# Kernel tuning notes

Measured on AMD Instinct MI355X. Metric: run time of the kernel, lower is better.

## Reference

```python
import jax, jax.numpy as jnp
import numpy as np
from jax import lax

B, C_IN, H, W = 16, 256, 64, 64
C_OUT, K_SZ, N_EXP, RED_C = 256, 3, 4, 16  # reduction_channels = max(256//16,16)=16


def setup_inputs() -> dict:
    key = jax.random.key(0)
    ks = jax.random.split(key, 6)
    x = jax.random.normal(ks[0], (B, C_IN, H, W), dtype=jnp.float32)
    # routing network params (1x1 convs == dense on pooled features)
    w1 = jax.random.normal(ks[1], (RED_C, C_IN), dtype=jnp.float32) * (1.0 / np.sqrt(C_IN))
    b1 = jnp.zeros((RED_C,), dtype=jnp.float32)
    w2 = jax.random.normal(ks[2], (N_EXP * C_IN, RED_C), dtype=jnp.float32) * (1.0 / np.sqrt(RED_C))
    b2 = jnp.zeros((N_EXP * C_IN,), dtype=jnp.float32)
    # expert weight bank (num_experts, c_out, c_in, kh, kw)
    fan_in = C_IN * K_SZ * K_SZ
    bound = np.sqrt(6.0 / fan_in)  # kaiming_uniform with a=sqrt(5) ~ U(-sqrt(6/fan_in)*..., simplified scale)
    weight = jax.random.uniform(ks[3], (N_EXP, C_OUT, C_IN, K_SZ, K_SZ), dtype=jnp.float32, minval=-bound, maxval=bound)
    return {"x": x, "w1": w1, "b1": b1, "w2": w2, "b2": b2, "weight": weight}


def reference(x, w1, b1, w2, b2, weight):
    b = x.shape[0]
    # route_func: global avg pool -> 1x1 conv -> relu -> 1x1 conv -> sigmoid
    pooled = jnp.mean(x, axis=(2, 3))                       # (b, c_in)
    r = jax.nn.relu(pooled @ w1.T + b1)                     # (b, red_c)
    rw = jax.nn.sigmoid(r @ w2.T + b2)                      # (b, K*c_in)
    rw = rw.reshape(b, N_EXP, C_IN)                         # (b, K, c_in)
    # per-sample combined kernel: sum over experts, routing scales input channels
    combined = jnp.einsum('bkc,kocij->bocij', rw, weight)   # (b, c_out, c_in, kh, kw)
    # per-sample conv (equivalent to groups=b trick in torch)
    def conv_one(xi, wi):
        return lax.conv_general_dilated(
            xi[None], wi, window_strides=(1, 1), padding=[(1, 1), (1, 1)],
            dimension_numbers=('NCHW', 'OIHW', 'NCHW'))[0]
    out = jax.vmap(conv_one)(x, combined)                   # (b, c_out, h, w)
    return out
```

## Files before the change

### kernel.cpp

```cpp
#include <hip/hip_runtime.h>
#include <hip/hip_bf16.h>
#include <math.h>

#define BB   16
#define CIN  256
#define HH   64
#define WW   64
#define COUT 256
#define NEXP 4
#define REDC 16
#define HW   (HH*WW)

typedef __attribute__((ext_vector_type(8))) short short8;
typedef __attribute__((ext_vector_type(16))) float f32x16;

#define AS1 __attribute__((address_space(1)))
#define AS3 __attribute__((address_space(3)))

__device__ __forceinline__ void gld_lds16(void* lds, const void* gp) {
    __builtin_amdgcn_global_load_lds((const AS1 unsigned int*)gp,
                                     (AS3 unsigned int*)lds, 16, 0, 0);
}

__global__ __launch_bounds__(256)
void transpose_pool_kernel(const float* __restrict__ x, ushort* __restrict__ xT,
                           float* __restrict__ pp) {
    int blk = blockIdx.x;
    int sq = blk & 3;
    int chunk = (blk >> 2) & 7;
    int b = blk >> 5;
    int c0 = chunk * 32;
    int s0 = sq * 1024;
    int tid = threadIdx.x;
    const float* xb = x + ((size_t)(b * CIN + c0)) * HW;
    ushort* xTb = xT + (size_t)b * HW * CIN;

    float psum[32];
    #pragma unroll
    for (int i = 0; i < 32; ++i) psum[i] = 0.f;

    for (int it = 0; it < 4; ++it) {
        int s = s0 + it * 256 + tid;
        unsigned int pk[16];
        #pragma unroll
        for (int p = 0; p < 16; ++p) {
            float lo = xb[(size_t)(2 * p) * HW + s];
            float hi = xb[(size_t)(2 * p + 1) * HW + s];
            psum[2 * p]     += lo;
            psum[2 * p + 1] += hi;
            asm volatile("v_cvt_pk_bf16_f32 %0, %1, %2" : "=v"(pk[p]) : "v"(lo), "v"(hi));
        }
        uint4* dst = (uint4*)(xTb + (size_t)s * CIN + c0);
        #pragma unroll
        for (int q = 0; q < 4; ++q)
            dst[q] = make_uint4(pk[q * 4], pk[q * 4 + 1], pk[q * 4 + 2], pk[q * 4 + 3]);
    }

    __shared__ float red[4][32];
    int lane = tid & 63, wid = tid >> 6;
    #pragma unroll
    for (int i = 0; i < 32; ++i) {
        float v = psum[i];
        #pragma unroll
        for (int off = 32; off > 0; off >>= 1) v += __shfl_down(v, off, 64);
        if (lane == 0) red[wid][i] = v;
    }
    __syncthreads();
    if (tid < 32)
        pp[(b * 4 + sq) * 256 + c0 + tid] = red[0][tid] + red[1][tid] + red[2][tid] + red[3][tid];
}

__global__ void route_kernel(const float* __restrict__ pp,
                             const float* __restrict__ w1, const float* __restrict__ b1,
                             const float* __restrict__ w2, const float* __restrict__ b2,
                             float* __restrict__ rw) {
    __shared__ float p_s[BB][CIN];
    __shared__ float r_s[BB][REDC];
    int tid = threadIdx.x;
    for (int i = tid; i < BB * CIN; i += 256) {
        int b = i >> 8, c = i & 255;
        p_s[b][c] = (pp[(b * 4 + 0) * 256 + c] + pp[(b * 4 + 1) * 256 + c] +
                     pp[(b * 4 + 2) * 256 + c] + pp[(b * 4 + 3) * 256 + c]) * (1.0f / HW);
    }
    __syncthreads();
    {
        int b = tid >> 4, j = tid & 15;
        float acc = b1[j];
        for (int c = 0; c < CIN; ++c) acc += p_s[b][c] * w1[j * CIN + c];
        r_s[b][j] = fmaxf(acc, 0.f);
    }
    __syncthreads();
    for (int i = tid; i < BB * NEXP * CIN; i += 256) {
        int b = i >> 10, o2 = i & 1023;
        float acc = b2[o2];
        #pragma unroll
        for (int j = 0; j < REDC; ++j) acc += r_s[b][j] * w2[o2 * REDC + j];
        rw[i] = 1.f / (1.f + expf(-acc));
    }
}

__global__ __launch_bounds__(256)
void combine3_kernel(const float* __restrict__ rw,
                     const float* __restrict__ weight,
                     ushort* __restrict__ cw) {
    int blk = blockIdx.x;
    int u = blk >> 1;
    int t = (blk & 1) * 256 + threadIdx.x;
    int gg = u & 1;
    int v = u >> 1;
    int t9 = v % 9;
    int cu = v / 9;
    int chunk16 = cu & 15;
    int ot = cu >> 4;
    int o_loc = t >> 3, c8 = t & 7;
    int o = ot * 64 + o_loc;
    int c = chunk16 * 16 + gg * 8 + c8;

    __shared__ float rw_s[16][4][8];
    int tid = threadIdx.x;
    #pragma unroll
    for (int r = 0; r < 2; ++r) {
        int i = r * 256 + tid;
        if (i < 512) {
            int b = i >> 5, k = (i >> 3) & 3, cc = i & 7;
            rw_s[b][k][cc] = rw[b * 1024 + k * 256 + chunk16 * 16 + gg * 8 + cc];
        }
    }
    __syncthreads();

    float wk0 = weight[((size_t)(0 * COUT + o) * CIN + c) * 9 + t9];
    float wk1 = weight[((size_t)(1 * COUT + o) * CIN + c) * 9 + t9];
    float wk2 = weight[((size_t)(2 * COUT + o) * CIN + c) * 9 + t9];
    float wk3 = weight[((size_t)(3 * COUT + o) * CIN + c) * 9 + t9];

    size_t base = (size_t)u * 512 + t;
    #pragma unroll
    for (int b = 0; b < 16; ++b) {
        float acc = rw_s[b][0][c8] * wk0 + rw_s[b][1][c8] * wk1 +
                    rw_s[b][2][c8] * wk2 + rw_s[b][3][c8] * wk3;
        __hip_bfloat16 hv = __float2bfloat16(acc);
        cw[base + (size_t)b * 589824] = *(ushort*)&hv;
    }
}

__global__ __launch_bounds__(512, 2)
void conv_mfma(const ushort* __restrict__ xT, const ushort* __restrict__ cw,
               float* __restrict__ out, const ushort* __restrict__ zp) {
    __shared__ ushort LDS[2][28672];

    int blk = blockIdx.x;
    int L = (blk & 7) * 32 + (blk >> 3);
    int b  = L >> 4;
    int rt = (L >> 2) & 3;
    int ot = L & 3;
    int r0 = rt * 16, o0 = ot * 64;
    int tid = threadIdx.x;
    int lane = tid & 63, wid = tid >> 6;
    int l31 = lane & 31, h = lane >> 5;

    f32x16 acc[2][4];
    #pragma unroll
    for (int mi = 0; mi < 2; ++mi)
        #pragma unroll
        for (int f = 0; f < 4; ++f) acc[mi][f] = (f32x16)0.f;

    const ushort* xTb = xT + (size_t)b * HW * CIN;
    const ushort* Ab  = cw + (size_t)((b * 4 + ot) * 16) * 9216;

    const char* srcb[7];
    int dsto[7];
    int strd[7];
    #pragma unroll
    for (int i = 0; i < 7; ++i) {
        int u = wid * 7 + i;
        if (u < 18) {
            srcb[i] = (const char*)(Ab + (size_t)u * 512 + lane * 8);
            dsto[i] = u * 1024;
            strd[i] = 18432;
        } else {
            int ux = u - 18;
            int half = ux & 1, u19 = ux >> 1;
            int s = u19 * 64 + lane;
            int r = (unsigned)s / 66u;
            int cc = s - r * 66;
            int grow = r0 - 1 + r;
            bool valid = (cc >= 1 && cc <= 64 && grow >= 0 && grow < 64 && s < 1188);
            srcb[i] = valid
                ? (const char*)(xTb + (size_t)(grow * 64 + cc - 1) * CIN + half * 8)
                : (const char*)(zp + lane * 8);
            dsto[i] = 18432 + half * 19456 + u19 * 1024;
            strd[i] = 32;
        }
    }

    char* ldsb = (char*)&LDS[0][0];

    #define STAGE(BUF, CH)                                                    \
    {                                                                         \
        _Pragma("unroll")                                                     \
        for (int i = 0; i < 7; ++i)                                           \
            gld_lds16(ldsb + (BUF) * 57344 + dsto[i],                         \
                      srcb[i] + (size_t)(CH) * strd[i]);                      \
    }

    #define LOADT(T, va0, va1, vb0, vb1, vb2, vb3)                            \
    {                                                                         \
        const int di_ = (T) / 3, dj_ = (T) - di_ * 3;                         \
        va0 = *(const short8*)&asb[(((T) * 2 + h) * 64 + 0  + l31) * 8];      \
        va1 = *(const short8*)&asb[(((T) * 2 + h) * 64 + 32 + l31) * 8];      \
        const int rr_ = wid * 2 + di_;                                        \
        vb0 = *(const short8*)&xsb[(rr_ * 66 +  0 + l31 + dj_) * 8];          \
        vb1 = *(const short8*)&xsb[(rr_ * 66 + 32 + l31 + dj_) * 8];          \
        vb2 = *(const short8*)&xsb[((rr_ + 1) * 66 +  0 + l31 + dj_) * 8];    \
        vb3 = *(const short8*)&xsb[((rr_ + 1) * 66 + 32 + l31 + dj_) * 8];    \
    }

    #define DOMM(va0, va1, vb0, vb1, vb2, vb3)                                          \
    {                                                                                   \
        acc[0][0] = __builtin_amdgcn_mfma_f32_32x32x16_bf16(va0, vb0, acc[0][0], 0,0,0);\
        acc[1][0] = __builtin_amdgcn_mfma_f32_32x32x16_bf16(va1, vb0, acc[1][0], 0,0,0);\
        acc[0][1] = __builtin_amdgcn_mfma_f32_32x32x16_bf16(va0, vb1, acc[0][1], 0,0,0);\
        acc[1][1] = __builtin_amdgcn_mfma_f32_32x32x16_bf16(va1, vb1, acc[1][1], 0,0,0);\
        acc[0][2] = __builtin_amdgcn_mfma_f32_32x32x16_bf16(va0, vb2, acc[0][2], 0,0,0);\
        acc[1][2] = __builtin_amdgcn_mfma_f32_32x32x16_bf16(va1, vb2, acc[1][2], 0,0,0);\
        acc[0][3] = __builtin_amdgcn_mfma_f32_32x32x16_bf16(va0, vb3, acc[0][3], 0,0,0);\
        acc[1][3] = __builtin_amdgcn_mfma_f32_32x32x16_bf16(va1, vb3, acc[1][3], 0,0,0);\
    }

    STAGE(0, 0)

    #pragma unroll 1
    for (int chunk = 0; chunk < 16; ++chunk) {
        int cur = chunk & 1;
        if (chunk < 15) {
            STAGE(cur ^ 1, chunk + 1)
            asm volatile("s_waitcnt vmcnt(7)" ::: "memory");
        } else {
            asm volatile("s_waitcnt vmcnt(0)" ::: "memory");
        }
        __builtin_amdgcn_s_barrier();
        __builtin_amdgcn_sched_barrier(0);

        const ushort* asb = &LDS[cur][0];
        const ushort* xsb = &LDS[cur][9216] + h * 9728;

        short8 a0A, a1A, b0A, b1A, b2A, b3A;
        short8 a0B, a1B, b0B, b1B, b2B, b3B;

        LOADT(0, a0A, a1A, b0A, b1A, b2A, b3A)
        LOADT(1, a0B, a1B, b0B, b1B, b2B, b3B)
        DOMM(a0A, a1A, b0A, b1A, b2A, b3A)
        LOADT(2, a0A, a1A, b0A, b1A, b2A, b3A)
        DOMM(a0B, a1B, b0B, b1B, b2B, b3B)
        LOADT(3, a0B, a1B, b0B, b1B, b2B, b3B)
        DOMM(a0A, a1A, b0A, b1A, b2A, b3A)
        LOADT(4, a0A, a1A, b0A, b1A, b2A, b3A)
        DOMM(a0B, a1B, b0B, b1B, b2B, b3B)
        LOADT(5, a0B, a1B, b0B, b1B, b2B, b3B)
        DOMM(a0A, a1A, b0A, b1A, b2A, b3A)
        LOADT(6, a0A, a1A, b0A, b1A, b2A, b3A)
        DOMM(a0B, a1B, b0B, b1B, b2B, b3B)
        LOADT(7, a0B, a1B, b0B, b1B, b2B, b3B)
        DOMM(a0A, a1A, b0A, b1A, b2A, b3A)
        LOADT(8, a0A, a1A, b0A, b1A, b2A, b3A)
        DOMM(a0B, a1B, b0B, b1B, b2B, b3B)
        DOMM(a0A, a1A, b0A, b1A, b2A, b3A)

        __builtin_amdgcn_sched_barrier(0);
        __builtin_amdgcn_s_barrier();
    }

    #pragma unroll
    for (int mi = 0; mi < 2; ++mi) {
        #pragma unroll
        for (int f = 0; f < 4; ++f) {
            int pos = (r0 + wid * 2 + (f >> 1)) * 64 + (f & 1) * 32 + l31;
            #pragma unroll
            for (int j = 0; j < 16; ++j) {
                int orow = (j & 3) + 8 * (j >> 2) + 4 * h;
                out[((size_t)(b * COUT + o0 + mi * 32 + orow)) * HW + pos] = acc[mi][f][j];
            }
        }
    }
    #undef STAGE
    #undef LOADT
    #undef DOMM
}

extern "C" void kernel_launch(void* const* d_in, const int* in_sizes, int n_in,
                              void* d_out, int out_size, void* d_ws, size_t ws_size,
                              hipStream_t stream) {
    const float* x      = (const float*)d_in[0];
    const float* w1     = (const float*)d_in[1];
    const float* b1     = (const float*)d_in[2];
    const float* w2     = (const float*)d_in[3];
    const float* b2     = (const float*)d_in[4];
    const float* weight = (const float*)d_in[5];
    float* out = (float*)d_out;

    float*  ws = (float*)d_ws;
    float*  pp = ws;
    float*  rw = ws + 16384;
    ushort* cw = (ushort*)(ws + 32768);
    ushort* xT = (ushort*)(ws + 32768 + 4718592);
    ushort* zp = xT + 16777216;

    hipMemsetAsync(zp, 0, 2048, stream);
    transpose_pool_kernel<<<512, 256, 0, stream>>>(x, xT, pp);
    route_kernel<<<1, 256, 0, stream>>>(pp, w1, b1, w2, b2, rw);
    combine3_kernel<<<2304, 256, 0, stream>>>(rw, weight, cw);
    conv_mfma<<<256, 512, 0, stream>>>(xT, cw, out, zp);
}
```

Baseline: 157.5 us.

## Store activations in channel-blocked layout for contiguous row loads into LDS

The transpose kernel now writes bf16 activations as [b][channel-block of 8][pixel][8] instead of pixel-major with all 256 channels, so each 64-pixel image row for one 8-channel slice is a contiguous 1 KB span. The conv kernel stages whole rows with one coalesced 16-byte-per-lane load, replacing the per-lane divide/modulo and scattered 32-byte-strided gathers. Padding columns are zeroed once in LDS up front, and the LDS buffer is resized to fit the new padded layout. In exchange it adds an initial LDS clear plus barrier, and it depends on padded halo slots never being overwritten.

```diff
diff --git a/kernel.cpp b/kernel.cpp
--- a/kernel.cpp
+++ b/kernel.cpp
@@ -33,7 +33,6 @@
     int s0 = sq * 1024;
     int tid = threadIdx.x;
     const float* xb = x + ((size_t)(b * CIN + c0)) * HW;
-    ushort* xTb = xT + (size_t)b * HW * CIN;
 
     float psum[32];
     #pragma unroll
@@ -50,10 +49,11 @@
             psum[2 * p + 1] += hi;
             asm volatile("v_cvt_pk_bf16_f32 %0, %1, %2" : "=v"(pk[p]) : "v"(lo), "v"(hi));
         }
-        uint4* dst = (uint4*)(xTb + (size_t)s * CIN + c0);
-        #pragma unroll
-        for (int q = 0; q < 4; ++q)
-            dst[q] = make_uint4(pk[q * 4], pk[q * 4 + 1], pk[q * 4 + 2], pk[q * 4 + 3]);
+        #pragma unroll
+        for (int q = 0; q < 4; ++q) {
+            ushort* dst = xT + ((size_t)(b * 32 + chunk * 4 + q) * HW + s) * 8;
+            *(uint4*)dst = make_uint4(pk[q * 4], pk[q * 4 + 1], pk[q * 4 + 2], pk[q * 4 + 3]);
+        }
     }
 
     __shared__ float red[4][32];
@@ -146,7 +146,7 @@
 __global__ __launch_bounds__(512, 2)
 void conv_mfma(const ushort* __restrict__ xT, const ushort* __restrict__ cw,
                float* __restrict__ out, const ushort* __restrict__ zp) {
-    __shared__ ushort LDS[2][28672];
+    __shared__ char LDS[2][57472];
 
     int blk = blockIdx.x;
     int L = (blk & 7) * 32 + (blk >> 3);
@@ -164,8 +164,8 @@
         #pragma unroll
         for (int f = 0; f < 4; ++f) acc[mi][f] = (f32x16)0.f;
 
-    const ushort* xTb = xT + (size_t)b * HW * CIN;
-    const ushort* Ab  = cw + (size_t)((b * 4 + ot) * 16) * 9216;
+    const char* xTb = (const char*)(xT + (size_t)b * 32 * HW * 8);
+    const ushort* Ab = cw + (size_t)((b * 4 + ot) * 16) * 9216;
 
     const char* srcb[7];
     int dsto[7];
@@ -174,32 +174,36 @@
     for (int i = 0; i < 7; ++i) {
         int u = wid * 7 + i;
         if (u < 18) {
-            srcb[i] = (const char*)(Ab + (size_t)u * 512 + lane * 8);
+            srcb[i] = (const char*)(Ab + (size_t)u * 512) + lane * 16;
             dsto[i] = u * 1024;
             strd[i] = 18432;
+        } else if (u < 54) {
+            int ux = u - 18;
+            int r = ux >> 1, half = ux & 1;
+            int grow = r0 - 1 + r;
+            bool valid = (grow >= 0 && grow < 64);
+            srcb[i] = valid
+                ? xTb + (size_t)(half * HW + grow * 64) * 16 + lane * 16
+                : (const char*)zp + lane * 16;
+            dsto[i] = 18432 + (half * 1188 + r * 66 + 1) * 16;
+            strd[i] = valid ? 131072 : 0;
         } else {
-            int ux = u - 18;
-            int half = ux & 1, u19 = ux >> 1;
-            int s = u19 * 64 + lane;
-            int r = (unsigned)s / 66u;
-            int cc = s - r * 66;
-            int grow = r0 - 1 + r;
-            bool valid = (cc >= 1 && cc <= 64 && grow >= 0 && grow < 64 && s < 1188);
-            srcb[i] = valid
-                ? (const char*)(xTb + (size_t)(grow * 64 + cc - 1) * CIN + half * 8)
-                : (const char*)(zp + lane * 8);
-            dsto[i] = 18432 + half * 19456 + u19 * 1024;
-            strd[i] = 32;
-        }
-    }
-
-    char* ldsb = (char*)&LDS[0][0];
+            srcb[i] = (const char*)zp + lane * 16;
+            dsto[i] = 56448;
+            strd[i] = 0;
+        }
+    }
+
+    char* ldsb = &LDS[0][0];
+
+    for (int i = tid; i < 28736; i += 512) ((unsigned int*)ldsb)[i] = 0;
+    __syncthreads();
 
     #define STAGE(BUF, CH)                                                    \
     {                                                                         \
         _Pragma("unroll")                                                     \
         for (int i = 0; i < 7; ++i)                                           \
-            gld_lds16(ldsb + (BUF) * 57344 + dsto[i],                         \
+            gld_lds16(ldsb + (BUF) * 57472 + dsto[i],                         \
                       srcb[i] + (size_t)(CH) * strd[i]);                      \
     }
 
@@ -241,8 +245,8 @@
         __builtin_amdgcn_s_barrier();
         __builtin_amdgcn_sched_barrier(0);
 
-        const ushort* asb = &LDS[cur][0];
-        const ushort* xsb = &LDS[cur][9216] + h * 9728;
+        const ushort* asb = (const ushort*)(ldsb + cur * 57472);
+        const ushort* xsb = (const ushort*)(ldsb + cur * 57472 + 18432) + h * 9504;
 
         short8 a0A, a1A, b0A, b1A, b2A, b3A;
         short8 a0B, a1B, b0B, b1B, b2B, b3B;
```

Result: faster. 143.2 us (-9.0%).
